# Performance work log

Measured on AMD Instinct MI355X. Metric: run time of the kernel, lower is better.

## Reference

```python
import jax, jax.numpy as jnp
import numpy as np

N, E, D, H, G = 50000, 600000, 128, 128, 128
NEG_SLOPE = 0.01
EPS = 1e-12


def _xavier(key, out_dim, in_dim):
    lim = float(np.sqrt(6.0 / (in_dim + out_dim)))
    return jax.random.uniform(key, (out_dim, in_dim), minval=-lim, maxval=lim, dtype=jnp.float32)


def setup_inputs() -> dict:
    key = jax.random.key(0)
    ks = jax.random.split(key, 12)
    x = jax.random.uniform(ks[0], (N, D), dtype=jnp.float32)
    edge_index = jax.random.randint(ks[1], (2, E), 0, N, dtype=jnp.int64)
    batch = jnp.sort(jax.random.randint(ks[2], (N,), 0, G, dtype=jnp.int64))
    return {
        "x": x,
        "edge_index": edge_index,
        "batch": batch,
        "W1l": _xavier(ks[3], H, D),
        "W1r": _xavier(ks[4], H, D),
        "W2l": _xavier(ks[5], H, H),
        "W2r": _xavier(ks[6], H, H),
        "fc1_W": _xavier(ks[7], H, H + D),
        "fc1_b": jnp.zeros((H,), jnp.float32),
        "fc2_W": _xavier(ks[8], H, H + H),
        "fc2_b": jnp.zeros((H,), jnp.float32),
        "fc3_W": _xavier(ks[9], H, H),
        "fc3_b": jnp.zeros((H,), jnp.float32),
    }


def _leaky(x):
    return jnp.where(x >= 0, x, NEG_SLOPE * x)


def _l2norm(x):
    # torch F.normalize(p=2, dim=-1) with eps clamp
    n = jnp.sqrt(jnp.sum(x * x, axis=-1, keepdims=True))
    return x / jnp.maximum(n, EPS)


def _sage_conv(x, src, dst, Wl, Wr):
    # PyG SAGEConv: out = lin_l(mean_{j in N(i)} x_j) + lin_r(x_i), L2-normalized
    msum = jax.ops.segment_sum(x[src], dst, num_segments=x.shape[0])  # [N, F]
    cnt = jax.ops.segment_sum(jnp.ones_like(dst, dtype=x.dtype), dst, num_segments=x.shape[0])
    mean = msum / jnp.maximum(cnt, 1.0)[:, None]
    out = mean @ Wl.T + x @ Wr.T
    return _l2norm(out)


def _preprocess(x):
    # row-normalize features (1/rowsum, inf -> 0)
    rs = jnp.sum(x, axis=1)
    rinv = jnp.where(rs == 0, 0.0, 1.0 / rs)
    return x * rinv[:, None]


def reference(x, edge_index, batch, W1l, W1r, W2l, W2r, fc1_W, fc1_b, fc2_W, fc2_b, fc3_W, fc3_b):
    src, dst = edge_index[0], edge_index[1]
    x = _preprocess(x)
    x_skip = x
    h = _leaky(_sage_conv(x, src, dst, W1l, W1r))
    h = jnp.concatenate([h, x_skip], axis=1)
    h = _leaky(h @ fc1_W.T + fc1_b)
    # double_layer=True
    h_skip = h
    h2 = _leaky(_sage_conv(h, src, dst, W2l, W2r))
    h2 = jnp.concatenate([h2, h_skip], axis=1)
    h = _leaky(h2 @ fc2_W.T + fc2_b)
    # global_add_pool over graphs
    pooled = jax.ops.segment_sum(h, batch, num_segments=G)  # [G, H]
    out = _leaky(pooled @ fc3_W.T + fc3_b)
    return _l2norm(out)
```

## Files before the change

### kernel.cpp

```cpp
#include <hip/hip_runtime.h>
#include <hip/hip_bf16.h>


#define NEG_SLOPE 0.01f
#define L2EPS 1e-12f

typedef unsigned short u16;
typedef short bf16x8 __attribute__((ext_vector_type(8)));
typedef short s16x4  __attribute__((ext_vector_type(4)));
typedef float f32x4  __attribute__((ext_vector_type(4)));

__device__ __forceinline__ float bf_lo(unsigned int u) {
    union { unsigned int i; float f; } v; v.i = u << 16; return v.f;
}
__device__ __forceinline__ float bf_hi(unsigned int u) {
    union { unsigned int i; float f; } v; v.i = u & 0xffff0000u; return v.f;
}
__device__ __forceinline__ u16 f2bf(float f) {
    union { float f; unsigned int i; } v; v.f = f;
    unsigned int r = v.i + 0x7fffu + ((v.i >> 16) & 1u);
    return (u16)(r >> 16);
}
__device__ __forceinline__ float bf2f(u16 u) {
    union { unsigned int i; float f; } v; v.i = ((unsigned int)u) << 16; return v.f;
}

__global__ void k_preprocess(const float* __restrict__ x, u16* __restrict__ xp, int N) {
    int node = blockIdx.x * 4 + (threadIdx.x >> 6);
    int lane = threadIdx.x & 63;
    if (node >= N) return;
    float2 v = ((const float2*)x)[(size_t)node * 64 + lane];
    float s = v.x + v.y;
    #pragma unroll
    for (int off = 32; off > 0; off >>= 1) s += __shfl_xor(s, off);
    float rinv = (s == 0.0f) ? 0.0f : 1.0f / s;
    unsigned int lo = f2bf(v.x * rinv), hi = f2bf(v.y * rinv);
    ((unsigned int*)xp)[(size_t)node * 64 + lane] = lo | (hi << 16);
}

__global__ void k_deg(const int* __restrict__ ei, int* __restrict__ deg, int E) {
    int e = blockIdx.x * blockDim.x + threadIdx.x;
    if (e >= E) return;
    atomicAdd(&deg[ei[E + e]], 1);
}

__global__ void k_scan_part(const int* __restrict__ deg, int* __restrict__ rs,
                            int* __restrict__ bsum, int N) {
    __shared__ int wsum[16];
    int t = threadIdx.x;
    int lane = t & 63, w = t >> 6;
    int i = blockIdx.x * 1024 + t;
    int v = (i < N) ? deg[i] : 0;
    int s = v;
    #pragma unroll
    for (int off = 1; off < 64; off <<= 1) {
        int u = __shfl_up(s, off);
        if (lane >= off) s += u;
    }
    if (lane == 63) wsum[w] = s;
    __syncthreads();
    if (w == 0) {
        int x = (lane < 16) ? wsum[lane] : 0;
        #pragma unroll
        for (int off = 1; off < 16; off <<= 1) {
            int u = __shfl_up(x, off);
            if (lane >= off) x += u;
        }
        if (lane < 16) wsum[lane] = x;
    }
    __syncthreads();
    int wexcl = (w == 0) ? 0 : wsum[w - 1];
    if (i < N) rs[i] = wexcl + s - v;
    if (t == 1023) bsum[blockIdx.x] = wexcl + s;
}

__global__ void k_scan_bsum(int* __restrict__ bsum, int* __restrict__ rs,
                            int nb, int N) {
    int lane = threadIdx.x;
    int v = (lane < nb) ? bsum[lane] : 0;
    int s = v;
    #pragma unroll
    for (int off = 1; off < 64; off <<= 1) {
        int u = __shfl_up(s, off);
        if (lane >= off) s += u;
    }
    if (lane < nb) bsum[lane] = s - v;
    if (lane == nb - 1) rs[N] = s;
}

__global__ void k_scan_add(int* __restrict__ rs, int* __restrict__ cursor,
                           const int* __restrict__ bsum, int N) {
    int i = blockIdx.x * 256 + threadIdx.x;
    if (i >= N) return;
    int v = rs[i] + bsum[i >> 10];
    rs[i] = v;
    cursor[i] = v;
}

__global__ void k_fill(const int* __restrict__ ei, int* __restrict__ cursor,
                       int* __restrict__ csr, int E) {
    int e = blockIdx.x * blockDim.x + threadIdx.x;
    if (e >= E) return;
    int src = ei[e];
    int dst = ei[E + e];
    int pos = atomicAdd(&cursor[dst], 1);
    csr[pos] = src;
}

__global__ void k_agg(const u16* __restrict__ feat, const int* __restrict__ csr,
                      const int* __restrict__ rs, u16* __restrict__ mean, int N) {
    int node = blockIdx.x * 4 + (threadIdx.x >> 6);
    int lane = threadIdx.x & 63;
    if (node >= N) return;
    int beg = rs[node], end = rs[node + 1];
    int d = end - beg;
    int q   = lane >> 4;
    int sub = lane & 15;
    const uint4* fp = (const uint4*)feat;
    float4 aA0 = {0.f,0.f,0.f,0.f}, aB0 = {0.f,0.f,0.f,0.f};
    float4 aA1 = {0.f,0.f,0.f,0.f}, aB1 = {0.f,0.f,0.f,0.f};
    int p = beg + q;
    for (; p + 4 < end; p += 8) {
        int s0 = csr[p], s1 = csr[p + 4];
        uint4 v0 = fp[(size_t)s0 * 16 + sub];
        uint4 v1 = fp[(size_t)s1 * 16 + sub];
        aA0.x += bf_lo(v0.x); aA0.y += bf_hi(v0.x);
        aA0.z += bf_lo(v0.y); aA0.w += bf_hi(v0.y);
        aB0.x += bf_lo(v0.z); aB0.y += bf_hi(v0.z);
        aB0.z += bf_lo(v0.w); aB0.w += bf_hi(v0.w);
        aA1.x += bf_lo(v1.x); aA1.y += bf_hi(v1.x);
        aA1.z += bf_lo(v1.y); aA1.w += bf_hi(v1.y);
        aB1.x += bf_lo(v1.z); aB1.y += bf_hi(v1.z);
        aB1.z += bf_lo(v1.w); aB1.w += bf_hi(v1.w);
    }
    if (p < end) {
        int s0 = csr[p];
        uint4 v0 = fp[(size_t)s0 * 16 + sub];
        aA0.x += bf_lo(v0.x); aA0.y += bf_hi(v0.x);
        aA0.z += bf_lo(v0.y); aA0.w += bf_hi(v0.y);
        aB0.x += bf_lo(v0.z); aB0.y += bf_hi(v0.z);
        aB0.z += bf_lo(v0.w); aB0.w += bf_hi(v0.w);
    }
    aA0.x += aA1.x; aA0.y += aA1.y; aA0.z += aA1.z; aA0.w += aA1.w;
    aB0.x += aB1.x; aB0.y += aB1.y; aB0.z += aB1.z; aB0.w += aB1.w;
    #pragma unroll
    for (int off = 16; off <= 32; off <<= 1) {
        aA0.x += __shfl_xor(aA0.x, off); aA0.y += __shfl_xor(aA0.y, off);
        aA0.z += __shfl_xor(aA0.z, off); aA0.w += __shfl_xor(aA0.w, off);
        aB0.x += __shfl_xor(aB0.x, off); aB0.y += __shfl_xor(aB0.y, off);
        aB0.z += __shfl_xor(aB0.z, off); aB0.w += __shfl_xor(aB0.w, off);
    }
    if (q == 0) {
        float inv = (d > 0) ? (1.0f / (float)d) : 0.0f;
        uint4 o;
        o.x = (unsigned int)f2bf(aA0.x * inv) | ((unsigned int)f2bf(aA0.y * inv) << 16);
        o.y = (unsigned int)f2bf(aA0.z * inv) | ((unsigned int)f2bf(aA0.w * inv) << 16);
        o.z = (unsigned int)f2bf(aB0.x * inv) | ((unsigned int)f2bf(aB0.y * inv) << 16);
        o.w = (unsigned int)f2bf(aB0.z * inv) | ((unsigned int)f2bf(aB0.w * inv) << 16);
        ((uint4*)mean)[(size_t)node * 16 + sub] = o;
    }
}

#define PK(lo_, hi_) ((unsigned int)f2bf(lo_) | ((unsigned int)f2bf(hi_) << 16))

#define LOAD_TILE(kb_) do {                                                    \
    const u16*   Asrc_ = ((kb_) < 4) ? A1 : A2;                                \
    const float* Wsrc_ = ((kb_) < 4) ? Wa : Wb;                                \
    int ldw_  = ((kb_) < 4) ? ldwa : ldwb;                                     \
    int kloc_ = ((kb_) & 3) * 32;                                              \
    int grow_ = i0 + a_row;                                                    \
    if (grow_ < N) sA = *(const uint4*)(Asrc_ + (size_t)grow_ * 128 + kloc_ + a_q * 8); \
    else           sA = make_uint4(0u, 0u, 0u, 0u);                            \
    const float* wp_ = Wsrc_ + (size_t)w_row * ldw_ + kloc_ + w_half * 16;     \
    sw0 = *(const float4*)(wp_);      sw1 = *(const float4*)(wp_ + 4);         \
    sw2 = *(const float4*)(wp_ + 8);  sw3 = *(const float4*)(wp_ + 12);        \
} while (0)

#define STORE_TILE() do {                                                      \
    *(uint4*)&Al[a_half][a_row][a_col0] = sA;                                  \
    uint4 wv_;                                                                 \
    wv_.x = PK(sw0.x, sw0.y); wv_.y = PK(sw0.z, sw0.w);                        \
    wv_.z = PK(sw1.x, sw1.y); wv_.w = PK(sw1.z, sw1.w);                        \
    *(uint4*)&Wl[w_half][w_row][0] = wv_;                                      \
    wv_.x = PK(sw2.x, sw2.y); wv_.y = PK(sw2.z, sw2.w);                        \
    wv_.z = PK(sw3.x, sw3.y); wv_.w = PK(sw3.z, sw3.w);                        \
    *(uint4*)&Wl[w_half][w_row][8] = wv_;                                      \
} while (0)

template <bool L2N, bool BIAS>
__global__ __launch_bounds__(256, 4) void k_gemm2(
    const u16* __restrict__ A1, const u16* __restrict__ A2,
    const float* __restrict__ Wa, int ldwa,
    const float* __restrict__ Wb, int ldwb,
    const float* __restrict__ bias,
    u16* __restrict__ out, int N)
{
    __shared__ u16 Al[2][64][40];
    __shared__ u16 Wl[2][128][40];
    int t = threadIdx.x;
    int i0 = blockIdx.x * 64;

    int a_row  = t >> 2;
    int a_q    = t & 3;
    int a_half = a_q >> 1;
    int a_col0 = (a_q & 1) * 8;
    int w_row  = t >> 1;
    int w_half = t & 1;

    int c16 = t & 15;
    int g   = (t >> 4) & 3;
    int wid = t >> 6;
    int ar  = wid * 16 + c16;
    int g4  = g * 4;

    f32x4 acc[8];
    #pragma unroll
    for (int cb = 0; cb < 8; ++cb) acc[cb] = (f32x4){0.f, 0.f, 0.f, 0.f};

    uint4 sA;
    float4 sw0, sw1, sw2, sw3;

    LOAD_TILE(0);

    union U8 { bf16x8 v; s16x4 h[2]; };

    for (int kb = 0; kb < 8; ++kb) {
        __syncthreads();
        STORE_TILE();
        __syncthreads();
        if (kb < 7) LOAD_TILE(kb + 1);

        U8 af;
        af.h[0] = *(const s16x4*)&Al[0][ar][g4];
        af.h[1] = *(const s16x4*)&Al[1][ar][g4];
        #pragma unroll
        for (int cb = 0; cb < 8; ++cb) {
            U8 bfr;
            int wr = cb * 16 + c16;
            bfr.h[0] = *(const s16x4*)&Wl[0][wr][g4];
            bfr.h[1] = *(const s16x4*)&Wl[1][wr][g4];
            acc[cb] = __builtin_amdgcn_mfma_f32_16x16x32_bf16(af.v, bfr.v, acc[cb], 0, 0, 0);
        }
    }

    float scs[4];
    if (L2N) {
        float s0 = 0.f, s1 = 0.f, s2 = 0.f, s3 = 0.f;
        #pragma unroll
        for (int cb = 0; cb < 8; ++cb) {
            s0 += acc[cb][0] * acc[cb][0];
            s1 += acc[cb][1] * acc[cb][1];
            s2 += acc[cb][2] * acc[cb][2];
            s3 += acc[cb][3] * acc[cb][3];
        }
        #pragma unroll
        for (int off = 1; off < 16; off <<= 1) {
            s0 += __shfl_xor(s0, off);
            s1 += __shfl_xor(s1, off);
            s2 += __shfl_xor(s2, off);
            s3 += __shfl_xor(s3, off);
        }
        scs[0] = 1.0f / fmaxf(sqrtf(s0), L2EPS);
        scs[1] = 1.0f / fmaxf(sqrtf(s1), L2EPS);
        scs[2] = 1.0f / fmaxf(sqrtf(s2), L2EPS);
        scs[3] = 1.0f / fmaxf(sqrtf(s3), L2EPS);
    }
    float bv[8];
    if (BIAS) {
        #pragma unroll
        for (int cb = 0; cb < 8; ++cb) bv[cb] = bias[cb * 16 + c16];
    }
    int rbase = i0 + wid * 16 + g * 4;
    #pragma unroll
    for (int reg = 0; reg < 4; ++reg) {
        int grow = rbase + reg;
        if (grow >= N) continue;
        #pragma unroll
        for (int cb = 0; cb < 8; ++cb) {
            float xv = acc[cb][reg];
            if (L2N) xv *= scs[reg];
            if (BIAS) xv += bv[cb];
            float r = (xv >= 0.f) ? xv : NEG_SLOPE * xv;
            out[(size_t)grow * 128 + cb * 16 + c16] = f2bf(r);
        }
    }
}

#define POOL_ROWS 128
__global__ void k_pool(const u16* __restrict__ h3, const int* __restrict__ batch,
                       float* __restrict__ pooled, int N) {
    int f = threadIdx.x;
    int base = blockIdx.x * POOL_ROWS;
    if (base >= N) return;
    int end = min(base + POOL_ROWS, N);
    float acc = 0.f;
    int cur = batch[base];
    for (int i = base; i < end; ++i) {
        int g = batch[i];
        if (g != cur) {
            atomicAdd(&pooled[cur * 128 + f], acc);
            acc = 0.f; cur = g;
        }
        acc += bf2f(h3[(size_t)i * 128 + f]);
    }
    atomicAdd(&pooled[cur * 128 + f], acc);
}

__global__ void k_fc3(const float* __restrict__ pooled, const float* __restrict__ W,
                      const float* __restrict__ b, float* __restrict__ out) {
    int g = blockIdx.x, f = threadIdx.x;
    __shared__ float prow[128];
    __shared__ float red[128];
    prow[f] = pooled[g * 128 + f];
    __syncthreads();
    float acc = b[f];
    #pragma unroll 8
    for (int k = 0; k < 128; ++k) acc += prow[k] * W[f * 128 + k];
    float v = (acc >= 0.f) ? acc : NEG_SLOPE * acc;
    red[f] = v * v;
    __syncthreads();
    for (int o = 64; o > 0; o >>= 1) {
        if (f < o) red[f] += red[f + o];
        __syncthreads();
    }
    float sc = 1.0f / fmaxf(sqrtf(red[0]), L2EPS);
    out[g * 128 + f] = v * sc;
}

extern "C" void kernel_launch(void* const* d_in, const int* in_sizes, int n_in,
                              void* d_out, int out_size, void* d_ws, size_t ws_size,
                              hipStream_t stream) {
    const float* x    = (const float*)d_in[0];
    const int*   ei   = (const int*)d_in[1];
    const int*   batch= (const int*)d_in[2];
    const float* W1l  = (const float*)d_in[3];
    const float* W1r  = (const float*)d_in[4];
    const float* W2l  = (const float*)d_in[5];
    const float* W2r  = (const float*)d_in[6];
    const float* fc1W = (const float*)d_in[7];
    const float* fc1b = (const float*)d_in[8];
    const float* fc2W = (const float*)d_in[9];
    const float* fc2b = (const float*)d_in[10];
    const float* fc3W = (const float*)d_in[11];
    const float* fc3b = (const float*)d_in[12];

    int N = in_sizes[0] / 128;
    int E = in_sizes[1] / 2;
    int G = out_size / 128;
    float* out = (float*)d_out;

    char* ws = (char*)d_ws;
    size_t off = 0;
    auto alloc = [&](size_t bytes) -> void* {
        void* p = ws + off;
        off = (off + bytes + 255) & ~(size_t)255;
        return p;
    };
    u16* xp     = (u16*)alloc((size_t)N * 128 * 2);
    u16* mean   = (u16*)alloc((size_t)N * 128 * 2);
    u16* h      = (u16*)alloc((size_t)N * 128 * 2);
    u16* h1     = (u16*)alloc((size_t)N * 128 * 2);
    float* pooled = (float*)alloc((size_t)G * 128 * 4);
    int* deg    = (int*)alloc((size_t)N * 4);
    int* rs     = (int*)alloc((size_t)(N + 1) * 4);
    int* cursor = (int*)alloc((size_t)N * 4);
    int* csr    = (int*)alloc((size_t)E * 4);
    int* bsum   = (int*)alloc(64 * 4);
    (void)ws_size; (void)n_in;

    hipMemsetAsync(deg, 0, (size_t)N * 4, stream);
    hipMemsetAsync(pooled, 0, (size_t)G * 128 * 4, stream);

    int nb = (N + 1023) / 1024;
    k_preprocess<<<(N + 3) / 4, 256, 0, stream>>>(x, xp, N);
    k_deg<<<(E + 255) / 256, 256, 0, stream>>>(ei, deg, E);
    k_scan_part<<<nb, 1024, 0, stream>>>(deg, rs, bsum, N);
    k_scan_bsum<<<1, 64, 0, stream>>>(bsum, rs, nb, N);
    k_scan_add<<<(N + 255) / 256, 256, 0, stream>>>(rs, cursor, bsum, N);
    k_fill<<<(E + 255) / 256, 256, 0, stream>>>(ei, cursor, csr, E);

    int gb = (N + 63) / 64;
    k_agg<<<(N + 3) / 4, 256, 0, stream>>>(xp, csr, rs, mean, N);
    k_gemm2<true, false><<<gb, 256, 0, stream>>>(
        mean, xp, W1l, 128, W1r, 128, nullptr, h, N);
    k_gemm2<false, true><<<gb, 256, 0, stream>>>(
        h, xp, fc1W, 256, fc1W + 128, 256, fc1b, h1, N);

    k_agg<<<(N + 3) / 4, 256, 0, stream>>>(h1, csr, rs, mean, N);
    k_gemm2<true, false><<<gb, 256, 0, stream>>>(
        mean, h1, W2l, 128, W2r, 128, nullptr, h, N);
    k_gemm2<false, true><<<gb, 256, 0, stream>>>(
        h, h1, fc2W, 256, fc2W + 128, 256, fc2b, xp, N);

    k_pool<<<(N + POOL_ROWS - 1) / POOL_ROWS, 128, 0, stream>>>(xp, batch, pooled, N);
    k_fc3<<<G, 128, 0, stream>>>(pooled, fc3W, fc3b, out);
}
```

Measured before the change: 327.5 us.

## Fuse SAGE conv GEMM with following FC GEMM and pre-convert weights to bf16

Merges each SAGE conv GEMM and the FC layer after it into one kernel. The L2-normalized, leaky-activated intermediate stays in shared memory instead of taking a bf16 round trip through global memory, and two launches per layer are removed. A new prologue kernel converts all weights to bf16 once, so the GEMM tile loads no longer convert from fp32. The cost is more shared memory per block and a lower occupancy bound (launch bounds go from 4 to 3), plus one extra small launch.

```diff
diff --git a/kernel.cpp b/kernel.cpp
--- a/kernel.cpp
+++ b/kernel.cpp
@@ -36,6 +36,28 @@
     float rinv = (s == 0.0f) ? 0.0f : 1.0f / s;
     unsigned int lo = f2bf(v.x * rinv), hi = f2bf(v.y * rinv);
     ((unsigned int*)xp)[(size_t)node * 64 + lane] = lo | (hi << 16);
+}
+
+__global__ void k_wconv(const float* __restrict__ W1l, const float* __restrict__ W1r,
+                        const float* __restrict__ W2l, const float* __restrict__ W2r,
+                        const float* __restrict__ f1,  const float* __restrict__ f2,
+                        u16* __restrict__ wbf) {
+    int i = blockIdx.x * 256 + threadIdx.x;
+    if (i >= 32768) return;
+    int e = i * 4;
+    const float* src; int off;
+    if (e < 65536) {
+        int m = e >> 14; off = e & 16383;
+        src = (m == 0) ? W1l : (m == 1) ? W1r : (m == 2) ? W2l : W2r;
+    } else {
+        int m = (e - 65536) >> 15; off = (e - 65536) & 32767;
+        src = (m == 0) ? f1 : f2;
+    }
+    float4 v = *(const float4*)(src + off);
+    uint2 o;
+    o.x = (unsigned int)f2bf(v.x) | ((unsigned int)f2bf(v.y) << 16);
+    o.y = (unsigned int)f2bf(v.z) | ((unsigned int)f2bf(v.w) << 16);
+    *(uint2*)(wbf + e) = o;
 }
 
 __global__ void k_deg(const int* __restrict__ ei, int* __restrict__ deg, int E) {
@@ -161,42 +183,45 @@
     }
 }
 
-#define PK(lo_, hi_) ((unsigned int)f2bf(lo_) | ((unsigned int)f2bf(hi_) << 16))
-
-#define LOAD_TILE(kb_) do {                                                    \
-    const u16*   Asrc_ = ((kb_) < 4) ? A1 : A2;                                \
-    const float* Wsrc_ = ((kb_) < 4) ? Wa : Wb;                                \
-    int ldw_  = ((kb_) < 4) ? ldwa : ldwb;                                     \
-    int kloc_ = ((kb_) & 3) * 32;                                              \
-    int grow_ = i0 + a_row;                                                    \
-    if (grow_ < N) sA = *(const uint4*)(Asrc_ + (size_t)grow_ * 128 + kloc_ + a_q * 8); \
-    else           sA = make_uint4(0u, 0u, 0u, 0u);                            \
-    const float* wp_ = Wsrc_ + (size_t)w_row * ldw_ + kloc_ + w_half * 16;     \
-    sw0 = *(const float4*)(wp_);      sw1 = *(const float4*)(wp_ + 4);         \
-    sw2 = *(const float4*)(wp_ + 8);  sw3 = *(const float4*)(wp_ + 12);        \
+
+#define LOAD_T1(kb_) do {                                                      \
+    const u16* As_ = ((kb_) < 4) ? Am : Ax;                                    \
+    const u16* Ws_ = ((kb_) < 4) ? Wlb : Wrb;                                  \
+    int kl_ = ((kb_) & 3) * 32;                                                \
+    int gr_ = i0 + a_row;                                                      \
+    if (gr_ < N) sA = *(const uint4*)(As_ + (size_t)gr_ * 128 + kl_ + a_q * 8);\
+    else         sA = make_uint4(0u, 0u, 0u, 0u);                              \
+    const u16* wp_ = Ws_ + (size_t)w_row * 128 + kl_ + w_half * 16;            \
+    sw0 = *(const uint4*)(wp_);  sw1 = *(const uint4*)(wp_ + 8);               \
 } while (0)
 
-#define STORE_TILE() do {                                                      \
-    *(uint4*)&Al[a_half][a_row][a_col0] = sA;                                  \
-    uint4 wv_;                                                                 \
-    wv_.x = PK(sw0.x, sw0.y); wv_.y = PK(sw0.z, sw0.w);                        \
-    wv_.z = PK(sw1.x, sw1.y); wv_.w = PK(sw1.z, sw1.w);                        \
-    *(uint4*)&Wl[w_half][w_row][0] = wv_;                                      \
-    wv_.x = PK(sw2.x, sw2.y); wv_.y = PK(sw2.z, sw2.w);                        \
-    wv_.z = PK(sw3.x, sw3.y); wv_.w = PK(sw3.z, sw3.w);                        \
-    *(uint4*)&Wl[w_half][w_row][8] = wv_;                                      \
+#define LOAD_T2(kb_) do {                                                      \
+    int kl_ = ((kb_) & 3) * 32;                                                \
+    if ((kb_) >= 4) {                                                          \
+        int gr_ = i0 + a_row;                                                  \
+        if (gr_ < N) sA = *(const uint4*)(Ax + (size_t)gr_ * 128 + kl_ + a_q * 8); \
+        else         sA = make_uint4(0u, 0u, 0u, 0u);                          \
+    }                                                                          \
+    int ko_ = kl_ + (((kb_) >= 4) ? 128 : 0);                                  \
+    const u16* wp_ = Wfb + (size_t)w_row * 256 + ko_ + w_half * 16;            \
+    sw0 = *(const uint4*)(wp_);  sw1 = *(const uint4*)(wp_ + 8);               \
 } while (0)
 
-template <bool L2N, bool BIAS>
-__global__ __launch_bounds__(256, 4) void k_gemm2(
-    const u16* __restrict__ A1, const u16* __restrict__ A2,
-    const float* __restrict__ Wa, int ldwa,
-    const float* __restrict__ Wb, int ldwb,
-    const float* __restrict__ bias,
+#define STORE_A() do { *(uint4*)&Al[a_half][a_row][a_col0] = sA; } while (0)
+#define STORE_W() do {                                                         \
+    *(uint4*)&Wl[w_half][w_row][0] = sw0;                                      \
+    *(uint4*)&Wl[w_half][w_row][8] = sw1;                                      \
+} while (0)
+
+__global__ __launch_bounds__(256, 3) void k_layer(
+    const u16* __restrict__ Am, const u16* __restrict__ Ax,
+    const u16* __restrict__ Wlb, const u16* __restrict__ Wrb,
+    const u16* __restrict__ Wfb, const float* __restrict__ bias,
     u16* __restrict__ out, int N)
 {
     __shared__ u16 Al[2][64][40];
     __shared__ u16 Wl[2][128][40];
+    __shared__ u16 hT[64][136];
     int t = threadIdx.x;
     int i0 = blockIdx.x * 64;
 
@@ -217,18 +242,15 @@
     #pragma unroll
     for (int cb = 0; cb < 8; ++cb) acc[cb] = (f32x4){0.f, 0.f, 0.f, 0.f};
 
-    uint4 sA;
-    float4 sw0, sw1, sw2, sw3;
-
-    LOAD_TILE(0);
-
+    uint4 sA, sw0, sw1;
     union U8 { bf16x8 v; s16x4 h[2]; };
 
+    LOAD_T1(0);
     for (int kb = 0; kb < 8; ++kb) {
         __syncthreads();
-        STORE_TILE();
+        STORE_A(); STORE_W();
         __syncthreads();
-        if (kb < 7) LOAD_TILE(kb + 1);
+        if (kb < 7) LOAD_T1(kb + 1);
 
         U8 af;
         af.h[0] = *(const s16x4*)&Al[0][ar][g4];
@@ -243,8 +265,7 @@
         }
     }
 
-    float scs[4];
-    if (L2N) {
+    {
         float s0 = 0.f, s1 = 0.f, s2 = 0.f, s3 = 0.f;
         #pragma unroll
         for (int cb = 0; cb < 8; ++cb) {
@@ -260,16 +281,55 @@
             s2 += __shfl_xor(s2, off);
             s3 += __shfl_xor(s3, off);
         }
+        float scs[4];
         scs[0] = 1.0f / fmaxf(sqrtf(s0), L2EPS);
         scs[1] = 1.0f / fmaxf(sqrtf(s1), L2EPS);
         scs[2] = 1.0f / fmaxf(sqrtf(s2), L2EPS);
         scs[3] = 1.0f / fmaxf(sqrtf(s3), L2EPS);
-    }
+        #pragma unroll
+        for (int reg = 0; reg < 4; ++reg) {
+            int rl = wid * 16 + g * 4 + reg;
+            #pragma unroll
+            for (int cb = 0; cb < 8; ++cb) {
+                float xv = acc[cb][reg] * scs[reg];
+                float r = (xv >= 0.f) ? xv : NEG_SLOPE * xv;
+                hT[rl][cb * 16 + c16] = f2bf(r);
+            }
+        }
+    }
+
+    #pragma unroll
+    for (int cb = 0; cb < 8; ++cb) acc[cb] = (f32x4){0.f, 0.f, 0.f, 0.f};
+
+    LOAD_T2(0);
+    for (int kb = 0; kb < 8; ++kb) {
+        __syncthreads();
+        if (kb >= 4) STORE_A();
+        STORE_W();
+        __syncthreads();
+        if (kb < 7) LOAD_T2(kb + 1);
+
+        U8 af;
+        if (kb < 4) {
+            af.h[0] = *(const s16x4*)&hT[ar][kb * 32 + g4];
+            af.h[1] = *(const s16x4*)&hT[ar][kb * 32 + 16 + g4];
+        } else {
+            af.h[0] = *(const s16x4*)&Al[0][ar][g4];
+            af.h[1] = *(const s16x4*)&Al[1][ar][g4];
+        }
+        #pragma unroll
+        for (int cb = 0; cb < 8; ++cb) {
+            U8 bfr;
+            int wr = cb * 16 + c16;
+            bfr.h[0] = *(const s16x4*)&Wl[0][wr][g4];
+            bfr.h[1] = *(const s16x4*)&Wl[1][wr][g4];
+            acc[cb] = __builtin_amdgcn_mfma_f32_16x16x32_bf16(af.v, bfr.v, acc[cb], 0, 0, 0);
+        }
+    }
+
     float bv[8];
-    if (BIAS) {
-        #pragma unroll
-        for (int cb = 0; cb < 8; ++cb) bv[cb] = bias[cb * 16 + c16];
-    }
+    #pragma unroll
+    for (int cb = 0; cb < 8; ++cb) bv[cb] = bias[cb * 16 + c16];
     int rbase = i0 + wid * 16 + g * 4;
     #pragma unroll
     for (int reg = 0; reg < 4; ++reg) {
@@ -277,9 +337,7 @@
         if (grow >= N) continue;
         #pragma unroll
         for (int cb = 0; cb < 8; ++cb) {
-            float xv = acc[cb][reg];
-            if (L2N) xv *= scs[reg];
-            if (BIAS) xv += bv[cb];
+            float xv = acc[cb][reg] + bv[cb];
             float r = (xv >= 0.f) ? xv : NEG_SLOPE * xv;
             out[(size_t)grow * 128 + cb * 16 + c16] = f2bf(r);
         }
@@ -358,8 +416,8 @@
     };
     u16* xp     = (u16*)alloc((size_t)N * 128 * 2);
     u16* mean   = (u16*)alloc((size_t)N * 128 * 2);
-    u16* h      = (u16*)alloc((size_t)N * 128 * 2);
     u16* h1     = (u16*)alloc((size_t)N * 128 * 2);
+    u16* wbf    = (u16*)alloc(131072 * 2);
     float* pooled = (float*)alloc((size_t)G * 128 * 4);
     int* deg    = (int*)alloc((size_t)N * 4);
     int* rs     = (int*)alloc((size_t)(N + 1) * 4);
@@ -373,6 +431,7 @@
 
     int nb = (N + 1023) / 1024;
     k_preprocess<<<(N + 3) / 4, 256, 0, stream>>>(x, xp, N);
+    k_wconv<<<128, 256, 0, stream>>>(W1l, W1r, W2l, W2r, fc1W, fc2W, wbf);
     k_deg<<<(E + 255) / 256, 256, 0, stream>>>(ei, deg, E);
     k_scan_part<<<nb, 1024, 0, stream>>>(deg, rs, bsum, N);
     k_scan_bsum<<<1, 64, 0, stream>>>(bsum, rs, nb, N);
@@ -381,16 +440,12 @@
 
     int gb = (N + 63) / 64;
     k_agg<<<(N + 3) / 4, 256, 0, stream>>>(xp, csr, rs, mean, N);
-    k_gemm2<true, false><<<gb, 256, 0, stream>>>(
-        mean, xp, W1l, 128, W1r, 128, nullptr, h, N);
-    k_gemm2<false, true><<<gb, 256, 0, stream>>>(
-        h, xp, fc1W, 256, fc1W + 128, 256, fc1b, h1, N);
+    k_layer<<<gb, 256, 0, stream>>>(
+        mean, xp, wbf, wbf + 16384, wbf + 65536, fc1b, h1, N);
 
     k_agg<<<(N + 3) / 4, 256, 0, stream>>>(h1, csr, rs, mean, N);
-    k_gemm2<true, false><<<gb, 256, 0, stream>>>(
-        mean, h1, W2l, 128, W2r, 128, nullptr, h, N);
-    k_gemm2<false, true><<<gb, 256, 0, stream>>>(
-        h, h1, fc2W, 256, fc2W + 128, 256, fc2b, xp, N);
+    k_layer<<<gb, 256, 0, stream>>>(
+        mean, h1, wbf + 32768, wbf + 49152, wbf + 98304, fc2b, xp, N);
 
     k_pool<<<(N + POOL_ROWS - 1) / POOL_ROWS, 128, 0, stream>>>(xp, batch, pooled, N);
     k_fc3<<<G, 128, 0, stream>>>(pooled, fc3W, fc3b, out);
```

After: 315.7 us. 3.6% less time.
